# Performance work log

Hardware: AMD Instinct MI355X
Metric: run time of the kernel (lower is better)

The kernel has to match this reference:

```python
import jax, jax.numpy as jnp
import numpy as np

N, F_IN, F_OUT = 8192, 256, 256
EDGE_PROB = 0.004  # avg degree ~33


def setup_inputs() -> dict:
    key = jax.random.key(0)
    k1, k2, k3, k4 = jax.random.split(key, 4)
    X = jax.random.normal(k1, (N, F_IN), dtype=jnp.float32)
    # binary adjacency (any nonzero entry in the original is an edge)
    adj = (jax.random.uniform(k2, (N, N)) < EDGE_PROB).astype(jnp.float32)
    W = jax.random.normal(k3, (F_OUT, F_IN), dtype=jnp.float32) * 0.05
    b = jnp.zeros((F_OUT,), dtype=jnp.float32)
    S = jax.random.normal(k4, (2 * F_OUT,), dtype=jnp.float32) * 0.05
    return {"X": X, "adj": adj, "W": W, "b": b, "S": S}


def reference(X, adj, W, b, S):
    # X: [N, F_in], adj: [N, N], W: [F_out, F_in], b: [F_out], S: [2*F_out]
    Xp = X @ W.T + b                      # [N, F_out]
    f = Xp.shape[1]
    n = X.shape[0]
    # per-edge score e_ij = leaky_relu(Xp_i . S[:f] + Xp_j . S[f:])
    a_src = Xp @ S[:f]                    # [N]
    a_dst = Xp @ S[f:]                    # [N]
    e = jax.nn.leaky_relu(a_src[:, None] + a_dst[None, :])  # [N, N]
    # edges = nonzero(adj + I): self-loops always present
    mask = (adj != 0) | jnp.eye(n, dtype=bool)
    e = jnp.where(mask, e, -jnp.inf)
    # local (per-source-node) softmax over neighbors == segment softmax on i
    attn = jax.nn.softmax(e, axis=1)      # [N, N]
    return jax.nn.sigmoid(attn @ Xp)      # [N, F_out]
```

## Files before the change

### kernel.cpp

```cpp
#include <hip/hip_runtime.h>
#include <math.h>

#define NN 8192
#define FF 256
#define MAXN 128

__global__ __launch_bounds__(256) void gemm_kernel(const float* __restrict__ X,
                                                   const float* __restrict__ W,
                                                   const float* __restrict__ bias,
                                                   float* __restrict__ Xp) {
    __shared__ float Xs[64][64];
    __shared__ float Ws[64][64];
    const int tid  = threadIdx.x;
    const int row0 = blockIdx.x * 64;
    const int col0 = blockIdx.y * 64;
    const int ty   = tid >> 4;
    const int tx   = tid & 15;
    const int lrow = tid & 63;
    const int kq0  = (tid >> 6) * 4;

    const float* Xr = &X[(size_t)(row0 + lrow) * FF];
    const float* Wr = &W[(size_t)(col0 + lrow) * FF];

    float4 px[4], pw[4];
#pragma unroll
    for (int q = 0; q < 4; ++q) {
        px[q] = *reinterpret_cast<const float4*>(&Xr[(kq0 + q) * 4]);
        pw[q] = *reinterpret_cast<const float4*>(&Wr[(kq0 + q) * 4]);
    }

    float acc[4][4] = {};

#pragma unroll
    for (int kt = 0; kt < 4; ++kt) {
#pragma unroll
        for (int q = 0; q < 4; ++q) {
            const int k0 = (kq0 + q) * 4;
            Xs[k0+0][lrow]=px[q].x; Xs[k0+1][lrow]=px[q].y; Xs[k0+2][lrow]=px[q].z; Xs[k0+3][lrow]=px[q].w;
            Ws[k0+0][lrow]=pw[q].x; Ws[k0+1][lrow]=pw[q].y; Ws[k0+2][lrow]=pw[q].z; Ws[k0+3][lrow]=pw[q].w;
        }
        __syncthreads();
        if (kt < 3) {
            const int kb = (kt + 1) * 64;
#pragma unroll
            for (int q = 0; q < 4; ++q) {
                px[q] = *reinterpret_cast<const float4*>(&Xr[kb + (kq0 + q) * 4]);
                pw[q] = *reinterpret_cast<const float4*>(&Wr[kb + (kq0 + q) * 4]);
            }
        }
#pragma unroll 8
        for (int k = 0; k < 64; ++k) {
            const float4 a4 = *reinterpret_cast<const float4*>(&Xs[k][ty * 4]);
            const float4 b4 = *reinterpret_cast<const float4*>(&Ws[k][tx * 4]);
            const float av[4] = {a4.x, a4.y, a4.z, a4.w};
            const float bv[4] = {b4.x, b4.y, b4.z, b4.w};
#pragma unroll
            for (int ii = 0; ii < 4; ++ii)
#pragma unroll
                for (int jj = 0; jj < 4; ++jj)
                    acc[ii][jj] = fmaf(av[ii], bv[jj], acc[ii][jj]);
        }
        __syncthreads();
    }

    const float4 b4 = *reinterpret_cast<const float4*>(&bias[col0 + tx * 4]);
#pragma unroll
    for (int ii = 0; ii < 4; ++ii) {
        const int r = row0 + ty * 4 + ii;
        float4 o;
        o.x = acc[ii][0] + b4.x;
        o.y = acc[ii][1] + b4.y;
        o.z = acc[ii][2] + b4.z;
        o.w = acc[ii][3] + b4.w;
        *reinterpret_cast<float4*>(&Xp[(size_t)r * FF + col0 + tx * 4]) = o;
    }
}

__global__ __launch_bounds__(256) void dots_kernel(const float* __restrict__ Xp,
                                                   const float* __restrict__ S,
                                                   float* __restrict__ a_src,
                                                   float* __restrict__ a_dst) {
    const int wid  = threadIdx.x >> 6;
    const int lane = threadIdx.x & 63;
    const int row  = blockIdx.x * 4 + wid;
    const float4 xv = *reinterpret_cast<const float4*>(&Xp[(size_t)row * FF + lane * 4]);
    const float4 s0 = *reinterpret_cast<const float4*>(&S[lane * 4]);
    const float4 s1 = *reinterpret_cast<const float4*>(&S[FF + lane * 4]);
    float ps = xv.x * s0.x + xv.y * s0.y + xv.z * s0.z + xv.w * s0.w;
    float pd = xv.x * s1.x + xv.y * s1.y + xv.z * s1.z + xv.w * s1.w;
#pragma unroll
    for (int off = 32; off; off >>= 1) {
        ps += __shfl_xor(ps, off);
        pd += __shfl_xor(pd, off);
    }
    if (lane == 0) {
        a_src[row] = ps;
        a_dst[row] = pd;
    }
}

__global__ __launch_bounds__(256) void csr_kernel(const float* __restrict__ adj,
                                                  const float* __restrict__ a_src,
                                                  const float* __restrict__ a_dst,
                                                  int* __restrict__ cnt_g,
                                                  int* __restrict__ nbr_g,
                                                  float* __restrict__ wt_g) {
    __shared__ int   nbr_s[MAXN];
    __shared__ float redm[4];
    __shared__ float reds[4];
    __shared__ int   cnt;

    const int i = blockIdx.x;
    const int t = threadIdx.x;
    if (t == 0) cnt = 0;
    __syncthreads();

    const size_t base = (size_t)i * NN;
#pragma unroll
    for (int it = 0; it < NN / 1024; ++it) {
        const int c0 = it * 1024 + t * 4;
        const float4 v = *reinterpret_cast<const float4*>(&adj[base + c0]);
        const float vv[4] = {v.x, v.y, v.z, v.w};
#pragma unroll
        for (int u = 0; u < 4; ++u) {
            const int col = c0 + u;
            if (vv[u] != 0.f || col == i) {
                const int slot = atomicAdd(&cnt, 1);
                if (slot < MAXN) nbr_s[slot] = col;
            }
        }
    }
    __syncthreads();

    const int n = min(cnt, MAXN);
    const float si = a_src[i];
    int   j  = 0;
    float ev = -INFINITY;
    if (t < n) {
        j = nbr_s[t];
        const float x = si + a_dst[j];
        ev = (x >= 0.f) ? x : 0.01f * x;
    }

    float m = ev;
#pragma unroll
    for (int off = 32; off; off >>= 1) m = fmaxf(m, __shfl_xor(m, off));
    if ((t & 63) == 0) redm[t >> 6] = m;
    __syncthreads();
    m = fmaxf(fmaxf(redm[0], redm[1]), fmaxf(redm[2], redm[3]));

    const float w = (t < n) ? __expf(ev - m) : 0.f;
    float s = w;
#pragma unroll
    for (int off = 32; off; off >>= 1) s += __shfl_xor(s, off);
    if ((t & 63) == 0) reds[t >> 6] = s;
    __syncthreads();
    const float inv_den = 1.f / (reds[0] + reds[1] + reds[2] + reds[3]);

    if (t < n) {
        nbr_g[(size_t)i * MAXN + t] = j;
        wt_g [(size_t)i * MAXN + t] = w * inv_den;
    }
    if (t == 0) cnt_g[i] = n;
}

__global__ __launch_bounds__(256) void agg_kernel(const int* __restrict__ cnt_g,
                                                  const int* __restrict__ nbr_g,
                                                  const float* __restrict__ wt_g,
                                                  const float* __restrict__ Xp,
                                                  float* __restrict__ out) {
    __shared__ int   nb[4][MAXN];
    __shared__ float wt[4][MAXN];

    const int wid  = threadIdx.x >> 6;
    const int lane = threadIdx.x & 63;
    const int i    = blockIdx.x * 4 + wid;

    const int n = cnt_g[i];
    if (lane < n) {
        nb[wid][lane] = nbr_g[(size_t)i * MAXN + lane];
        wt[wid][lane] = wt_g [(size_t)i * MAXN + lane];
    }
    if (lane + 64 < n) {
        nb[wid][lane + 64] = nbr_g[(size_t)i * MAXN + lane + 64];
        wt[wid][lane + 64] = wt_g [(size_t)i * MAXN + lane + 64];
    }
    __syncthreads();

    const float* xb = Xp + lane * 4;
    float4 acc = {0.f, 0.f, 0.f, 0.f};
    int k = 0;
    for (; k + 2 <= n; k += 2) {
        const int   j0 = nb[wid][k],     j1 = nb[wid][k + 1];
        const float w0 = wt[wid][k],     w1 = wt[wid][k + 1];
        const float4 v0 = *reinterpret_cast<const float4*>(&xb[(size_t)j0 * FF]);
        const float4 v1 = *reinterpret_cast<const float4*>(&xb[(size_t)j1 * FF]);
        acc.x += w0 * v0.x + w1 * v1.x;
        acc.y += w0 * v0.y + w1 * v1.y;
        acc.z += w0 * v0.z + w1 * v1.z;
        acc.w += w0 * v0.w + w1 * v1.w;
    }
    if (k < n) {
        const int   j0 = nb[wid][k];
        const float w0 = wt[wid][k];
        const float4 v0 = *reinterpret_cast<const float4*>(&xb[(size_t)j0 * FF]);
        acc.x += w0 * v0.x; acc.y += w0 * v0.y; acc.z += w0 * v0.z; acc.w += w0 * v0.w;
    }

    float4 o;
    o.x = 1.f / (1.f + __expf(-acc.x));
    o.y = 1.f / (1.f + __expf(-acc.y));
    o.z = 1.f / (1.f + __expf(-acc.z));
    o.w = 1.f / (1.f + __expf(-acc.w));
    *reinterpret_cast<float4*>(&out[(size_t)i * FF + lane * 4]) = o;
}

extern "C" void kernel_launch(void* const* d_in, const int* in_sizes, int n_in,
                              void* d_out, int out_size, void* d_ws, size_t ws_size,
                              hipStream_t stream) {
    const float* X   = (const float*)d_in[0];
    const float* adj = (const float*)d_in[1];
    const float* W   = (const float*)d_in[2];
    const float* b   = (const float*)d_in[3];
    const float* S   = (const float*)d_in[4];
    float* out = (float*)d_out;

    float* Xp    = (float*)d_ws;
    float* a_src = Xp + (size_t)NN * FF;
    float* a_dst = a_src + NN;
    int*   cnt_g = (int*)(a_dst + NN);
    int*   nbr_g = cnt_g + NN;
    float* wt_g  = (float*)(nbr_g + (size_t)NN * MAXN);

    gemm_kernel<<<dim3(NN / 64, FF / 64), 256, 0, stream>>>(X, W, b, Xp);
    dots_kernel<<<NN / 4, 256, 0, stream>>>(Xp, S, a_src, a_dst);
    csr_kernel<<<NN, 256, 0, stream>>>(adj, a_src, a_dst, cnt_g, nbr_g, wt_g);
    agg_kernel<<<NN / 4, 256, 0, stream>>>(cnt_g, nbr_g, wt_g, Xp, out);
}
```

Baseline: 413.8 us.

## Overlap adjacency scan with GEMM and fuse softmax into aggregation

Merges the GEMM and the adjacency-row neighbor scan into one launch with separate block roles, since neighbor extraction does not depend on the projected features. Softmax scoring moves into the aggregation kernel, so the per-edge weight buffer is no longer written and reread. The scan also batches all row loads before processing. This trades a larger heterogeneous grid and more work per wave in aggregation for one fewer launch and overlap of the bandwidth-bound scan with compute.

```diff
diff --git a/kernel.cpp b/kernel.cpp
--- a/kernel.cpp
+++ b/kernel.cpp
@@ -4,75 +4,114 @@
 #define NN 8192
 #define FF 256
 #define MAXN 128
-
-__global__ __launch_bounds__(256) void gemm_kernel(const float* __restrict__ X,
-                                                   const float* __restrict__ W,
-                                                   const float* __restrict__ bias,
-                                                   float* __restrict__ Xp) {
+#define NGEMM ((NN / 64) * (FF / 64))
+
+__global__ __launch_bounds__(256) void gemm_scan_kernel(const float* __restrict__ X,
+                                                        const float* __restrict__ W,
+                                                        const float* __restrict__ bias,
+                                                        const float* __restrict__ adj,
+                                                        float* __restrict__ Xp,
+                                                        int* __restrict__ cnt_g,
+                                                        int* __restrict__ nbr_g) {
     __shared__ float Xs[64][64];
     __shared__ float Ws[64][64];
-    const int tid  = threadIdx.x;
-    const int row0 = blockIdx.x * 64;
-    const int col0 = blockIdx.y * 64;
-    const int ty   = tid >> 4;
-    const int tx   = tid & 15;
-    const int lrow = tid & 63;
-    const int kq0  = (tid >> 6) * 4;
-
-    const float* Xr = &X[(size_t)(row0 + lrow) * FF];
-    const float* Wr = &W[(size_t)(col0 + lrow) * FF];
-
-    float4 px[4], pw[4];
-#pragma unroll
-    for (int q = 0; q < 4; ++q) {
-        px[q] = *reinterpret_cast<const float4*>(&Xr[(kq0 + q) * 4]);
-        pw[q] = *reinterpret_cast<const float4*>(&Wr[(kq0 + q) * 4]);
-    }
-
-    float acc[4][4] = {};
-
-#pragma unroll
-    for (int kt = 0; kt < 4; ++kt) {
+    __shared__ int   nbr_s[MAXN];
+    __shared__ int   cnt;
+
+    const int tid = threadIdx.x;
+
+    if (blockIdx.x < NGEMM) {
+        const int rt   = blockIdx.x >> 2;
+        const int ct   = blockIdx.x & 3;
+        const int row0 = rt * 64;
+        const int col0 = ct * 64;
+        const int ty   = tid >> 4;
+        const int tx   = tid & 15;
+        const int lrow = tid & 63;
+        const int kq0  = (tid >> 6) * 4;
+
+        const float* Xr = &X[(size_t)(row0 + lrow) * FF];
+        const float* Wr = &W[(size_t)(col0 + lrow) * FF];
+
+        float4 px[4], pw[4];
 #pragma unroll
         for (int q = 0; q < 4; ++q) {
-            const int k0 = (kq0 + q) * 4;
-            Xs[k0+0][lrow]=px[q].x; Xs[k0+1][lrow]=px[q].y; Xs[k0+2][lrow]=px[q].z; Xs[k0+3][lrow]=px[q].w;
-            Ws[k0+0][lrow]=pw[q].x; Ws[k0+1][lrow]=pw[q].y; Ws[k0+2][lrow]=pw[q].z; Ws[k0+3][lrow]=pw[q].w;
-        }
+            px[q] = *reinterpret_cast<const float4*>(&Xr[(kq0 + q) * 4]);
+            pw[q] = *reinterpret_cast<const float4*>(&Wr[(kq0 + q) * 4]);
+        }
+
+        float acc[4][4] = {};
+
+#pragma unroll
+        for (int kt = 0; kt < 4; ++kt) {
+#pragma unroll
+            for (int q = 0; q < 4; ++q) {
+                const int k0 = (kq0 + q) * 4;
+                Xs[k0+0][lrow]=px[q].x; Xs[k0+1][lrow]=px[q].y; Xs[k0+2][lrow]=px[q].z; Xs[k0+3][lrow]=px[q].w;
+                Ws[k0+0][lrow]=pw[q].x; Ws[k0+1][lrow]=pw[q].y; Ws[k0+2][lrow]=pw[q].z; Ws[k0+3][lrow]=pw[q].w;
+            }
+            __syncthreads();
+            if (kt < 3) {
+                const int kb = (kt + 1) * 64;
+#pragma unroll
+                for (int q = 0; q < 4; ++q) {
+                    px[q] = *reinterpret_cast<const float4*>(&Xr[kb + (kq0 + q) * 4]);
+                    pw[q] = *reinterpret_cast<const float4*>(&Wr[kb + (kq0 + q) * 4]);
+                }
+            }
+#pragma unroll 8
+            for (int k = 0; k < 64; ++k) {
+                const float4 a4 = *reinterpret_cast<const float4*>(&Xs[k][ty * 4]);
+                const float4 b4 = *reinterpret_cast<const float4*>(&Ws[k][tx * 4]);
+                const float av[4] = {a4.x, a4.y, a4.z, a4.w};
+                const float bv[4] = {b4.x, b4.y, b4.z, b4.w};
+#pragma unroll
+                for (int ii = 0; ii < 4; ++ii)
+#pragma unroll
+                    for (int jj = 0; jj < 4; ++jj)
+                        acc[ii][jj] = fmaf(av[ii], bv[jj], acc[ii][jj]);
+            }
+            __syncthreads();
+        }
+
+        const float4 b4 = *reinterpret_cast<const float4*>(&bias[col0 + tx * 4]);
+#pragma unroll
+        for (int ii = 0; ii < 4; ++ii) {
+            const int r = row0 + ty * 4 + ii;
+            float4 o;
+            o.x = acc[ii][0] + b4.x;
+            o.y = acc[ii][1] + b4.y;
+            o.z = acc[ii][2] + b4.z;
+            o.w = acc[ii][3] + b4.w;
+            *reinterpret_cast<float4*>(&Xp[(size_t)r * FF + col0 + tx * 4]) = o;
+        }
+    } else {
+        const int i = blockIdx.x - NGEMM;
+        if (tid == 0) cnt = 0;
         __syncthreads();
-        if (kt < 3) {
-            const int kb = (kt + 1) * 64;
-#pragma unroll
-            for (int q = 0; q < 4; ++q) {
-                px[q] = *reinterpret_cast<const float4*>(&Xr[kb + (kq0 + q) * 4]);
-                pw[q] = *reinterpret_cast<const float4*>(&Wr[kb + (kq0 + q) * 4]);
-            }
-        }
-#pragma unroll 8
-        for (int k = 0; k < 64; ++k) {
-            const float4 a4 = *reinterpret_cast<const float4*>(&Xs[k][ty * 4]);
-            const float4 b4 = *reinterpret_cast<const float4*>(&Ws[k][tx * 4]);
-            const float av[4] = {a4.x, a4.y, a4.z, a4.w};
-            const float bv[4] = {b4.x, b4.y, b4.z, b4.w};
-#pragma unroll
-            for (int ii = 0; ii < 4; ++ii)
-#pragma unroll
-                for (int jj = 0; jj < 4; ++jj)
-                    acc[ii][jj] = fmaf(av[ii], bv[jj], acc[ii][jj]);
+
+        const size_t base = (size_t)i * NN;
+        float4 v[8];
+#pragma unroll
+        for (int it = 0; it < 8; ++it)
+            v[it] = *reinterpret_cast<const float4*>(&adj[base + it * 1024 + tid * 4]);
+#pragma unroll
+        for (int it = 0; it < 8; ++it) {
+            const int c0 = it * 1024 + tid * 4;
+            const float vv[4] = {v[it].x, v[it].y, v[it].z, v[it].w};
+#pragma unroll
+            for (int u = 0; u < 4; ++u) {
+                const int col = c0 + u;
+                if (vv[u] != 0.f || col == i) {
+                    const int slot = atomicAdd(&cnt, 1);
+                    if (slot < MAXN) nbr_s[slot] = col;
+                }
+            }
         }
         __syncthreads();
-    }
-
-    const float4 b4 = *reinterpret_cast<const float4*>(&bias[col0 + tx * 4]);
-#pragma unroll
-    for (int ii = 0; ii < 4; ++ii) {
-        const int r = row0 + ty * 4 + ii;
-        float4 o;
-        o.x = acc[ii][0] + b4.x;
-        o.y = acc[ii][1] + b4.y;
-        o.z = acc[ii][2] + b4.z;
-        o.w = acc[ii][3] + b4.w;
-        *reinterpret_cast<float4*>(&Xp[(size_t)r * FF + col0 + tx * 4]) = o;
+        const int n = min(cnt, MAXN);
+        if (tid < n) nbr_g[(size_t)i * MAXN + tid] = nbr_s[tid];
+        if (tid == 0) cnt_g[i] = n;
     }
 }
 
@@ -99,74 +138,10 @@
     }
 }
 
-__global__ __launch_bounds__(256) void csr_kernel(const float* __restrict__ adj,
+__global__ __launch_bounds__(256) void agg_kernel(const int* __restrict__ cnt_g,
+                                                  const int* __restrict__ nbr_g,
                                                   const float* __restrict__ a_src,
                                                   const float* __restrict__ a_dst,
-                                                  int* __restrict__ cnt_g,
-                                                  int* __restrict__ nbr_g,
-                                                  float* __restrict__ wt_g) {
-    __shared__ int   nbr_s[MAXN];
-    __shared__ float redm[4];
-    __shared__ float reds[4];
-    __shared__ int   cnt;
-
-    const int i = blockIdx.x;
-    const int t = threadIdx.x;
-    if (t == 0) cnt = 0;
-    __syncthreads();
-
-    const size_t base = (size_t)i * NN;
-#pragma unroll
-    for (int it = 0; it < NN / 1024; ++it) {
-        const int c0 = it * 1024 + t * 4;
-        const float4 v = *reinterpret_cast<const float4*>(&adj[base + c0]);
-        const float vv[4] = {v.x, v.y, v.z, v.w};
-#pragma unroll
-        for (int u = 0; u < 4; ++u) {
-            const int col = c0 + u;
-            if (vv[u] != 0.f || col == i) {
-                const int slot = atomicAdd(&cnt, 1);
-                if (slot < MAXN) nbr_s[slot] = col;
-            }
-        }
-    }
-    __syncthreads();
-
-    const int n = min(cnt, MAXN);
-    const float si = a_src[i];
-    int   j  = 0;
-    float ev = -INFINITY;
-    if (t < n) {
-        j = nbr_s[t];
-        const float x = si + a_dst[j];
-        ev = (x >= 0.f) ? x : 0.01f * x;
-    }
-
-    float m = ev;
-#pragma unroll
-    for (int off = 32; off; off >>= 1) m = fmaxf(m, __shfl_xor(m, off));
-    if ((t & 63) == 0) redm[t >> 6] = m;
-    __syncthreads();
-    m = fmaxf(fmaxf(redm[0], redm[1]), fmaxf(redm[2], redm[3]));
-
-    const float w = (t < n) ? __expf(ev - m) : 0.f;
-    float s = w;
-#pragma unroll
-    for (int off = 32; off; off >>= 1) s += __shfl_xor(s, off);
-    if ((t & 63) == 0) reds[t >> 6] = s;
-    __syncthreads();
-    const float inv_den = 1.f / (reds[0] + reds[1] + reds[2] + reds[3]);
-
-    if (t < n) {
-        nbr_g[(size_t)i * MAXN + t] = j;
-        wt_g [(size_t)i * MAXN + t] = w * inv_den;
-    }
-    if (t == 0) cnt_g[i] = n;
-}
-
-__global__ __launch_bounds__(256) void agg_kernel(const int* __restrict__ cnt_g,
-                                                  const int* __restrict__ nbr_g,
-                                                  const float* __restrict__ wt_g,
                                                   const float* __restrict__ Xp,
                                                   float* __restrict__ out) {
     __shared__ int   nb[4][MAXN];
@@ -176,35 +151,57 @@
     const int lane = threadIdx.x & 63;
     const int i    = blockIdx.x * 4 + wid;
 
-    const int n = cnt_g[i];
+    const int   n  = cnt_g[i];
+    const float si = a_src[i];
+
+    int   j0 = 0, j1 = 0;
+    float e0 = -INFINITY, e1 = -INFINITY;
     if (lane < n) {
-        nb[wid][lane] = nbr_g[(size_t)i * MAXN + lane];
-        wt[wid][lane] = wt_g [(size_t)i * MAXN + lane];
+        j0 = nbr_g[(size_t)i * MAXN + lane];
+        const float x = si + a_dst[j0];
+        e0 = (x >= 0.f) ? x : 0.01f * x;
     }
     if (lane + 64 < n) {
-        nb[wid][lane + 64] = nbr_g[(size_t)i * MAXN + lane + 64];
-        wt[wid][lane + 64] = wt_g [(size_t)i * MAXN + lane + 64];
-    }
+        j1 = nbr_g[(size_t)i * MAXN + lane + 64];
+        const float x = si + a_dst[j1];
+        e1 = (x >= 0.f) ? x : 0.01f * x;
+    }
+
+    float m = fmaxf(e0, e1);
+#pragma unroll
+    for (int off = 32; off; off >>= 1) m = fmaxf(m, __shfl_xor(m, off));
+
+    const float w0 = (lane < n)      ? __expf(e0 - m) : 0.f;
+    const float w1 = (lane + 64 < n) ? __expf(e1 - m) : 0.f;
+    float s = w0 + w1;
+#pragma unroll
+    for (int off = 32; off; off >>= 1) s += __shfl_xor(s, off);
+    const float inv_den = 1.f / s;
+
+    nb[wid][lane]      = j0;
+    wt[wid][lane]      = w0 * inv_den;
+    nb[wid][lane + 64] = j1;
+    wt[wid][lane + 64] = w1 * inv_den;
     __syncthreads();
 
     const float* xb = Xp + lane * 4;
     float4 acc = {0.f, 0.f, 0.f, 0.f};
     int k = 0;
     for (; k + 2 <= n; k += 2) {
-        const int   j0 = nb[wid][k],     j1 = nb[wid][k + 1];
-        const float w0 = wt[wid][k],     w1 = wt[wid][k + 1];
-        const float4 v0 = *reinterpret_cast<const float4*>(&xb[(size_t)j0 * FF]);
-        const float4 v1 = *reinterpret_cast<const float4*>(&xb[(size_t)j1 * FF]);
-        acc.x += w0 * v0.x + w1 * v1.x;
-        acc.y += w0 * v0.y + w1 * v1.y;
-        acc.z += w0 * v0.z + w1 * v1.z;
-        acc.w += w0 * v0.w + w1 * v1.w;
+        const int   g0 = nb[wid][k],     g1 = nb[wid][k + 1];
+        const float u0 = wt[wid][k],     u1 = wt[wid][k + 1];
+        const float4 v0 = *reinterpret_cast<const float4*>(&xb[(size_t)g0 * FF]);
+        const float4 v1 = *reinterpret_cast<const float4*>(&xb[(size_t)g1 * FF]);
+        acc.x += u0 * v0.x + u1 * v1.x;
+        acc.y += u0 * v0.y + u1 * v1.y;
+        acc.z += u0 * v0.z + u1 * v1.z;
+        acc.w += u0 * v0.w + u1 * v1.w;
     }
     if (k < n) {
-        const int   j0 = nb[wid][k];
-        const float w0 = wt[wid][k];
-        const float4 v0 = *reinterpret_cast<const float4*>(&xb[(size_t)j0 * FF]);
-        acc.x += w0 * v0.x; acc.y += w0 * v0.y; acc.z += w0 * v0.z; acc.w += w0 * v0.w;
+        const int   g0 = nb[wid][k];
+        const float u0 = wt[wid][k];
+        const float4 v0 = *reinterpret_cast<const float4*>(&xb[(size_t)g0 * FF]);
+        acc.x += u0 * v0.x; acc.y += u0 * v0.y; acc.z += u0 * v0.z; acc.w += u0 * v0.w;
     }
 
     float4 o;
@@ -230,10 +227,8 @@
     float* a_dst = a_src + NN;
     int*   cnt_g = (int*)(a_dst + NN);
     int*   nbr_g = cnt_g + NN;
-    float* wt_g  = (float*)(nbr_g + (size_t)NN * MAXN);
-
-    gemm_kernel<<<dim3(NN / 64, FF / 64), 256, 0, stream>>>(X, W, b, Xp);
+
+    gemm_scan_kernel<<<NGEMM + NN, 256, 0, stream>>>(X, W, b, adj, Xp, cnt_g, nbr_g);
     dots_kernel<<<NN / 4, 256, 0, stream>>>(Xp, S, a_src, a_dst);
-    csr_kernel<<<NN, 256, 0, stream>>>(adj, a_src, a_dst, cnt_g, nbr_g, wt_g);
-    agg_kernel<<<NN / 4, 256, 0, stream>>>(cnt_g, nbr_g, wt_g, Xp, out);
-}
+    agg_kernel<<<NN / 4, 256, 0, stream>>>(cnt_g, nbr_g, a_src, a_dst, Xp, out);
+}
```

New measurement: 398.4 us. 1.04x faster.
